# Kernel tuning notes

Measured on AMD Instinct MI355X. Metric: run time of the kernel, lower is better.

The kernel has to match this reference:

```python
import jax, jax.numpy as jnp
import numpy as np

HEAD_SIZE = 64
N_EMBD = 768

def setup_inputs() -> dict:
    key = jax.random.key(0)
    k1, k2, k3, k4 = jax.random.split(key, 4)
    x = jax.random.normal(k1, (8, 2048, N_EMBD), dtype=jnp.float32)
    # nn.Linear weights are [out, in]; we store transposed [in, out] for x @ W
    scale = 1.0 / np.sqrt(N_EMBD)
    Wk = jax.random.uniform(k2, (N_EMBD, HEAD_SIZE), jnp.float32, -scale, scale)
    Wq = jax.random.uniform(k3, (N_EMBD, HEAD_SIZE), jnp.float32, -scale, scale)
    Wv = jax.random.uniform(k4, (N_EMBD, HEAD_SIZE), jnp.float32, -scale, scale)
    return {"x": x, "Wk": Wk, "Wq": Wq, "Wv": Wv}

def reference(x, Wk, Wq, Wv):
    # x: [B, T, C]
    k = x @ Wk  # [B, T, H]
    q = x @ Wq  # [B, T, H]
    v = x @ Wv  # [B, T, H]
    inv_sqrt_h = jnp.asarray(k.shape[-1], x.dtype) ** -0.5
    att = jnp.einsum('bth,bsh->bts', q, k) * inv_sqrt_h  # [B, T, T]
    att = jax.nn.softmax(att, axis=-1)  # no causal mask in original
    out = jnp.einsum('bts,bsh->bth', att, v)  # [B, T, H]
    return out
```

## Files before the change

### kernel.cpp

```cpp
#include <hip/hip_runtime.h>
#include <hip/hip_bf16.h>


#define SEQ   2048
#define CEMB  768
#define SCL 0.18033688011112042f
#define THR 11.0f

typedef __attribute__((ext_vector_type(4))) float f32x4;
typedef __attribute__((ext_vector_type(4))) float fvec4;
typedef __attribute__((ext_vector_type(8))) short short8;
typedef __attribute__((ext_vector_type(4))) short short4v;
typedef __attribute__((ext_vector_type(4))) unsigned short u16x4;
typedef __attribute__((ext_vector_type(8))) unsigned short u16x8;
typedef __attribute__((ext_vector_type(2))) unsigned int u32x2;

#define MFMA32 __builtin_amdgcn_mfma_f32_16x16x32_bf16

__device__ __forceinline__ unsigned short f2bf(float f) {
    unsigned int u = __builtin_bit_cast(unsigned int, f);
    u += 0x7fffu + ((u >> 16) & 1u);
    return (unsigned short)(u >> 16);
}
__device__ __forceinline__ float bf2f(unsigned short s) {
    return __builtin_bit_cast(float, (unsigned int)s << 16);
}
__device__ __forceinline__ unsigned int pack_bf2(float lo, float hi) {
    unsigned int ulo = __builtin_bit_cast(unsigned int, lo);
    unsigned int uhi = __builtin_bit_cast(unsigned int, hi);
    return ((uhi + 0x8000u) & 0xffff0000u) | ((ulo + 0x8000u) >> 16);
}
__device__ __forceinline__ short8 pack8(fvec4 a, fvec4 b) {
    short8 s;
    #pragma unroll
    for (int j = 0; j < 4; ++j) {
        s[j]     = (short)f2bf(a[j]);
        s[4 + j] = (short)f2bf(b[j]);
    }
    return s;
}
__device__ __forceinline__ f32x4 vmax4(f32x4 a, f32x4 b) {
    f32x4 r;
    r[0] = fmaxf(a[0], b[0]); r[1] = fmaxf(a[1], b[1]);
    r[2] = fmaxf(a[2], b[2]); r[3] = fmaxf(a[3], b[3]);
    return r;
}
__device__ __forceinline__ void gl_lds16(const void* g, void* l) {
    __builtin_amdgcn_global_load_lds(
        (const __attribute__((address_space(1))) unsigned int*)g,
        (__attribute__((address_space(3))) unsigned int*)l, 16, 0, 0);
}

__global__ void wt_kernel(const float* __restrict__ Wq, const float* __restrict__ Wk,
                          const float* __restrict__ Wv, unsigned short* __restrict__ wt) {
    int idx = blockIdx.x * 256 + threadIdx.x;
    int o = idx / 49152;
    int r = idx % 49152;
    int n = r / 768;
    int k = r % 768;
    const float* W = (o == 0) ? Wq : (o == 1) ? Wk : Wv;
    wt[idx] = f2bf(W[k * 64 + n]);
}

__global__ __launch_bounds__(768) void proj_kernel(
        const float* __restrict__ x, const unsigned short* __restrict__ wt,
        unsigned short* __restrict__ qg, unsigned short* __restrict__ kg,
        unsigned short* __restrict__ vtg) {
    __shared__ __align__(16) unsigned short xl[2][12288];

    const int tid = threadIdx.x;
    const int lane = tid & 63;
    const int wv = tid >> 6;
    const int l15 = lane & 15;
    const int lq = lane >> 4;
    const int o = wv >> 2;
    const int f = wv & 3;
    const int rowbase = blockIdx.x * 64;

    short8 wfr[24];
    #pragma unroll
    for (int s = 0; s < 24; ++s)
        wfr[s] = *reinterpret_cast<const short8*>(
            &wt[o * 49152 + (f * 16 + l15) * CEMB + s * 32 + lq * 8]);

    const int S0 = tid, S1 = 768 + tid;
    const int r0 = S0 / 96, c0 = S0 - r0 * 96;
    const int r1 = S1 / 96, c1 = S1 - r1 * 96;
    const int d0 = r0 * 1536 + ((c0 ^ (r0 & 7)) << 4);
    const int d1 = r1 * 1536 + ((c1 ^ (r1 & 7)) << 4);

    #define LOADT(PA0, PA1, PB0, PB1, T) do {                               \
        const float* g0_ = x + (size_t)(rowbase + (T) * 16 + r0) * CEMB + c0 * 8; \
        const float* g1_ = x + (size_t)(rowbase + (T) * 16 + r1) * CEMB + c1 * 8; \
        PA0 = *reinterpret_cast<const fvec4*>(g0_);                         \
        PA1 = *reinterpret_cast<const fvec4*>(g0_ + 4);                     \
        PB0 = *reinterpret_cast<const fvec4*>(g1_);                         \
        PB1 = *reinterpret_cast<const fvec4*>(g1_ + 4);                     \
    } while (0)

    fvec4 pb[2][4];
    {
        fvec4 a0, a1, b0, b1;
        LOADT(a0, a1, b0, b1, 0);
        *reinterpret_cast<short8*>((char*)&xl[0][0] + d0) = pack8(a0, a1);
        *reinterpret_cast<short8*>((char*)&xl[0][0] + d1) = pack8(b0, b1);
        LOADT(pb[0][0], pb[0][1], pb[0][2], pb[0][3], 1);
    }
    __syncthreads();

    #pragma unroll
    for (int t = 0; t < 4; ++t) {
        const int cur = t & 1;
        if (t < 2)
            LOADT(pb[cur ^ 1][0], pb[cur ^ 1][1], pb[cur ^ 1][2], pb[cur ^ 1][3], t + 2);

        f32x4 acc = f32x4{0.f, 0.f, 0.f, 0.f};
        const char* xb = (const char*)&xl[cur][0];
        const int rswz = l15 & 7;
        #pragma unroll
        for (int s = 0; s < 24; ++s) {
            short8 bf = *reinterpret_cast<const short8*>(
                xb + l15 * 1536 + (((s * 4 + lq) ^ rswz) << 4));
            acc = MFMA32(wfr[s], bf, acc, 0, 0, 0);
        }

        if (t < 3) {
            *reinterpret_cast<short8*>((char*)&xl[cur ^ 1][0] + d0) =
                pack8(pb[cur][0], pb[cur][1]);
            *reinterpret_cast<short8*>((char*)&xl[cur ^ 1][0] + d1) =
                pack8(pb[cur][2], pb[cur][3]);
        }

        const int xrow = rowbase + t * 16 + l15;
        if (o < 2) {
            const float sc = o ? 1.f : SCL;
            u16x4 st;
            #pragma unroll
            for (int r = 0; r < 4; ++r) st[r] = f2bf(acc[r] * sc);
            unsigned short* dst = (o ? kg : qg) + (size_t)xrow * 64 + f * 16 + lq * 4;
            *reinterpret_cast<u16x4*>(dst) = st;
        } else {
            const int bb = xrow >> 11;
            const int tt = xrow & 2047;
            #pragma unroll
            for (int r = 0; r < 4; ++r)
                vtg[(size_t)bb * 131072 + (size_t)(f * 16 + lq * 4 + r) * SEQ + tt] =
                    f2bf(acc[r]);
        }
        __syncthreads();
    }
    #undef LOADT
}

#if __has_builtin(__builtin_amdgcn_mfma_f32_16x16x16bf16_1k)
#define HAVE_MFMA16 1
#define MFMA16 __builtin_amdgcn_mfma_f32_16x16x16bf16_1k
#else
#define HAVE_MFMA16 0
#endif

__global__ __launch_bounds__(256) void attn_kernel(
        const unsigned short* __restrict__ qg, const unsigned short* __restrict__ kg,
        const unsigned short* __restrict__ vtg, unsigned short* __restrict__ pO,
        float* __restrict__ pm, float* __restrict__ pl) {
    __shared__ __align__(16) unsigned short kbuf[2][4096];
    __shared__ __align__(16) unsigned short vbuf[2][4096];

    const int tid = threadIdx.x;
    const int lane = tid & 63;
    const int wv = tid >> 6;
    const int l15 = lane & 15;
    const int lq = lane >> 4;

    const int swz = (blockIdx.x & 7) * 64 + (blockIdx.x >> 3);
    const int b = swz >> 6;
    const int qt = (swz >> 2) & 15;
    const int ks = swz & 3;
    const int qrow0 = b * SEQ + qt * 128 + wv * 32;

    const unsigned short* kgb = kg + (size_t)(b * SEQ + ks * 512) * 64;
    const unsigned short* vgb = vtg + (size_t)b * 131072 + ks * 512;

    const int sr0 = tid >> 3;
    const int sw0 = (((tid & 7) ^ (sr0 & 7)) * 8);
    const int sr1 = 32 + sr0;
    const int sw1 = (((tid & 7) ^ (sr1 & 7)) * 8);
    #define STAGE(S, KT) do {                                                        \
        gl_lds16(kgb + (size_t)((KT) * 64 + sr0) * 64 + sw0, &kbuf[S][tid * 8]);       \
        gl_lds16(kgb + (size_t)((KT) * 64 + sr1) * 64 + sw1, &kbuf[S][2048 + tid * 8]); \
        gl_lds16(vgb + (size_t)sr0 * SEQ + (KT) * 64 + sw0, &vbuf[S][tid * 8]);        \
        gl_lds16(vgb + (size_t)sr1 * SEQ + (KT) * 64 + sw1, &vbuf[S][2048 + tid * 8]);  \
    } while (0)

    const short8 bq00 = *reinterpret_cast<const short8*>(&qg[(size_t)(qrow0 + l15) * 64 + lq * 8]);
    const short8 bq01 = *reinterpret_cast<const short8*>(&qg[(size_t)(qrow0 + l15) * 64 + 32 + lq * 8]);
    const short8 bq10 = *reinterpret_cast<const short8*>(&qg[(size_t)(qrow0 + 16 + l15) * 64 + lq * 8]);
    const short8 bq11 = *reinterpret_cast<const short8*>(&qg[(size_t)(qrow0 + 16 + l15) * 64 + 32 + lq * 8]);

    f32x4 acc0[4], acc1[4];
    #pragma unroll
    for (int hb = 0; hb < 4; ++hb) {
        acc0[hb] = f32x4{0.f, 0.f, 0.f, 0.f};
        acc1[hb] = f32x4{0.f, 0.f, 0.f, 0.f};
    }
    float m0 = -3e38f, m1 = -3e38f, l0 = 0.f, l1 = 0.f;

    STAGE(0, 0);
    __syncthreads();

    #define SUBITER(BQ0, BQ1, MM, LL, ACC) do {                                      \
        f32x4 st[4];                                                                 \
        _Pragma("unroll")                                                            \
        for (int kb = 0; kb < 4; ++kb) {                                             \
            f32x4 z = {0.f, 0.f, 0.f, 0.f};                                          \
            st[kb] = MFMA32(kf[2 * kb], BQ0, z, 0, 0, 0);                            \
            st[kb] = MFMA32(kf[2 * kb + 1], BQ1, st[kb], 0, 0, 0);                   \
        }                                                                            \
        f32x4 mx = vmax4(vmax4(st[0], st[1]), vmax4(st[2], st[3]));                  \
        float p = fmaxf(fmaxf(mx[0], mx[1]), fmaxf(mx[2], mx[3]));                   \
        p = fmaxf(p, __shfl_xor(p, 16)); p = fmaxf(p, __shfl_xor(p, 32));            \
        if (__any(p > MM + THR)) {                                                   \
            float mn = fmaxf(MM, p);                                                 \
            float al = exp2f(MM - mn);                                               \
            MM = mn; LL *= al;                                                       \
            _Pragma("unroll")                                                        \
            for (int hb = 0; hb < 4; ++hb)                                           \
                _Pragma("unroll")                                                    \
                for (int r = 0; r < 4; ++r) ACC[hb][r] *= al;                        \
        }                                                                            \
        unsigned int w[4][2];                                                        \
        _Pragma("unroll")                                                            \
        for (int kb = 0; kb < 4; ++kb) {                                             \
            float e0 = exp2f(st[kb][0] - MM), e1 = exp2f(st[kb][1] - MM);            \
            float e2 = exp2f(st[kb][2] - MM), e3 = exp2f(st[kb][3] - MM);            \
            LL += (e0 + e1) + (e2 + e3);                                             \
            w[kb][0] = pack_bf2(e0, e1); w[kb][1] = pack_bf2(e2, e3);                \
        }                                                                            \
        PVACC_L(w, ACC);                                                             \
    } while (0)

#if HAVE_MFMA16
    #define PVLOAD_L                                                                 \
        short4v va[16];                                                              \
        _Pragma("unroll")                                                            \
        for (int hb = 0; hb < 4; ++hb) {                                             \
            const int row = hb * 16 + l15, rs = row & 7, rb = row * 128;             \
            _Pragma("unroll")                                                        \
            for (int kb = 0; kb < 4; ++kb)                                           \
                va[hb * 4 + kb] = *reinterpret_cast<const short4v*>(                 \
                    vb_ + rb + (((kb * 2 + (lq >> 1)) ^ rs) << 4) + (lq & 1) * 8);   \
        }
    #define PVACC_L(W, ACC) do {                                                     \
        _Pragma("unroll")                                                            \
        for (int hb = 0; hb < 4; ++hb) {                                             \
            f32x4 a = ACC[hb];                                                       \
            _Pragma("unroll")                                                        \
            for (int kb = 0; kb < 4; ++kb) {                                         \
                u32x2 uv; uv[0] = W[kb][0]; uv[1] = W[kb][1];                        \
                a = MFMA16(va[hb * 4 + kb], __builtin_bit_cast(short4v, uv), a, 0, 0, 0); \
            }                                                                        \
            ACC[hb] = a;                                                             \
        }                                                                            \
    } while (0)
#else
    #define PVLOAD_L                                                                 \
        short8 va[8];                                                                \
        _Pragma("unroll")                                                            \
        for (int hb = 0; hb < 4; ++hb) {                                             \
            const int row = hb * 16 + l15, rs = row & 7, rb = row * 128;             \
            _Pragma("unroll")                                                        \
            for (int h = 0; h < 2; ++h)                                              \
                va[hb * 2 + h] = *reinterpret_cast<const short8*>(                   \
                    vb_ + rb + (((h * 4 + lq) ^ rs) << 4));                          \
        }
    #define PVACC_L(W, ACC) do {                                                     \
        _Pragma("unroll")                                                            \
        for (int h = 0; h < 2; ++h) {                                                \
            unsigned int bw0, bw1, bw2, bw3;                                         \
            {                                                                        \
                int src0 = l15 + (((lq & 1) * 2) << 4);                              \
                int src1 = l15 + ((((lq & 1) * 2) + 1) << 4);                        \
                unsigned int a0 = (unsigned int)__shfl((int)W[h * 2][0], src0);      \
                unsigned int a1 = (unsigned int)__shfl((int)W[h * 2 + 1][0], src0);  \
                unsigned int b0 = (unsigned int)__shfl((int)W[h * 2][1], src0);      \
                unsigned int b1 = (unsigned int)__shfl((int)W[h * 2 + 1][1], src0);  \
                unsigned int c0_ = (unsigned int)__shfl((int)W[h * 2][0], src1);     \
                unsigned int c1_ = (unsigned int)__shfl((int)W[h * 2 + 1][0], src1); \
                unsigned int d0_ = (unsigned int)__shfl((int)W[h * 2][1], src1);     \
                unsigned int d1_ = (unsigned int)__shfl((int)W[h * 2 + 1][1], src1); \
                bw0 = (lq >> 1) ? a1 : a0; bw1 = (lq >> 1) ? b1 : b0;                \
                bw2 = (lq >> 1) ? c1_ : c0_; bw3 = (lq >> 1) ? d1_ : d0_;            \
            }                                                                        \
            short8 bp;                                                               \
            {                                                                        \
                unsigned int t_[4] = {bw0, bw2, bw1, bw3};                           \
                bp = *reinterpret_cast<short8*>(t_);                                 \
            }                                                                        \
            _Pragma("unroll")                                                        \
            for (int hb = 0; hb < 4; ++hb)                                           \
                ACC[hb] = MFMA32(va[hb * 2 + h], bp, ACC[hb], 0, 0, 0);              \
        }                                                                            \
    } while (0)
#endif

    #define ITERL(S) do {                                                            \
        const char* kb_ = (const char*)&kbuf[S][0];                                  \
        const char* vb_ = (const char*)&vbuf[S][0];                                  \
        short8 kf[8];                                                                \
        _Pragma("unroll")                                                            \
        for (int kb = 0; kb < 4; ++kb) {                                             \
            const int row = kb * 16 + l15, rs = row & 7, rb = row * 128;             \
            kf[2 * kb]     = *reinterpret_cast<const short8*>(kb_ + rb + ((lq ^ rs) << 4));       \
            kf[2 * kb + 1] = *reinterpret_cast<const short8*>(kb_ + rb + (((lq + 4) ^ rs) << 4)); \
        }                                                                            \
        PVLOAD_L;                                                                    \
        SUBITER(bq00, bq01, m0, l0, acc0);                                           \
        SUBITER(bq10, bq11, m1, l1, acc1);                                           \
    } while (0)

    #pragma unroll
    for (int kt2 = 0; kt2 < 4; ++kt2) {
        const int t0 = kt2 * 2;
        if (t0 + 1 < 8) STAGE(1, t0 + 1);
        ITERL(0);
        __syncthreads();
        if (t0 + 2 < 8) STAGE(0, t0 + 2);
        ITERL(1);
        __syncthreads();
    }

    l0 += __shfl_xor(l0, 16); l0 += __shfl_xor(l0, 32);
    l1 += __shfl_xor(l1, 16); l1 += __shfl_xor(l1, 32);

    #pragma unroll
    for (int s = 0; s < 2; ++s) {
        const int q = qrow0 + s * 16 + l15;
        f32x4* ac = s ? acc1 : acc0;
        #pragma unroll
        for (int hb = 0; hb < 4; ++hb) {
            u16x4 st;
            #pragma unroll
            for (int r = 0; r < 4; ++r) st[r] = f2bf(ac[hb][r]);
            *reinterpret_cast<u16x4*>(&pO[((size_t)(ks * 16384 + q)) * 64 + hb * 16 + lq * 4]) = st;
        }
        pm[ks * 16384 + q] = s ? m1 : m0;
        pl[ks * 16384 + q] = s ? l1 : l0;
    }
    #undef STAGE
    #undef ITERL
    #undef SUBITER
    #undef PVLOAD_L
    #undef PVACC_L
}

__global__ __launch_bounds__(256) void combine_kernel(
        float* __restrict__ out, const unsigned short* __restrict__ pO,
        const float* __restrict__ pm, const float* __restrict__ pl) {
    const int idx = blockIdx.x * 256 + threadIdx.x;
    const int q = idx >> 2;
    const int c0 = (idx & 3) * 16;

    float mv[4], lv[4];
    #pragma unroll
    for (int k = 0; k < 4; ++k) {
        mv[k] = pm[k * 16384 + q];
        lv[k] = pl[k * 16384 + q];
    }
    float M = fmaxf(fmaxf(mv[0], mv[1]), fmaxf(mv[2], mv[3]));
    float e[4], L = 0.f;
    #pragma unroll
    for (int k = 0; k < 4; ++k) {
        e[k] = exp2f(mv[k] - M);
        L += lv[k] * e[k];
    }
    const float inv = 1.0f / L;

    float res[16];
    #pragma unroll
    for (int j = 0; j < 16; ++j) res[j] = 0.f;
    #pragma unroll
    for (int k = 0; k < 4; ++k) {
        const unsigned short* p = &pO[((size_t)(k * 16384 + q)) * 64 + c0];
        u16x8 a = *reinterpret_cast<const u16x8*>(p);
        u16x8 b = *reinterpret_cast<const u16x8*>(p + 8);
        #pragma unroll
        for (int j = 0; j < 8; ++j) {
            res[j]     += e[k] * bf2f(a[j]);
            res[8 + j] += e[k] * bf2f(b[j]);
        }
    }
    float* op = &out[(size_t)q * 64 + c0];
    #pragma unroll
    for (int v = 0; v < 4; ++v) {
        fvec4 r;
        #pragma unroll
        for (int j = 0; j < 4; ++j) r[j] = res[v * 4 + j] * inv;
        *reinterpret_cast<fvec4*>(op + v * 4) = r;
    }
}

extern "C" void kernel_launch(void* const* d_in, const int* in_sizes, int n_in,
                              void* d_out, int out_size, void* d_ws, size_t ws_size,
                              hipStream_t stream) {
    (void)in_sizes; (void)n_in; (void)out_size; (void)ws_size;
    const float* x  = (const float*)d_in[0];
    const float* Wk = (const float*)d_in[1];
    const float* Wq = (const float*)d_in[2];
    const float* Wv = (const float*)d_in[3];
    float* out = (float*)d_out;

    unsigned short* ws = (unsigned short*)d_ws;
    unsigned short* qg  = ws;
    unsigned short* kg  = ws + 1048576;
    unsigned short* vtg = ws + 2097152;
    unsigned short* wt  = ws + 3145728;
    float* pm = (float*)((char*)d_ws + 6586368);
    float* pl = pm + 65536;
    unsigned short* pO = (unsigned short*)((char*)d_ws + 7110656);

    wt_kernel<<<576, 256, 0, stream>>>(Wq, Wk, Wv, wt);
    proj_kernel<<<256, 768, 0, stream>>>(x, wt, qg, kg, vtg);
    attn_kernel<<<512, 256, 0, stream>>>(qg, kg, vtg, pO, pm, pl);
    combine_kernel<<<256, 256, 0, stream>>>(out, pO, pm, pl);
}
```

Before: 55.11 us.

## Fuse weight conversion into projection and split-K combine into attention kernel

Removes the separate weight-transpose kernel: each projection block now loads the fp32 weights directly with strided scalar reads and converts them to bf16 in registers. It also removes the separate combine kernel. The last of the four key-split attention blocks for each query tile, found with an atomic counter and threadfences, merges the partial outputs in place. This saves two kernel launches and their inter-kernel gaps, at the cost of uncoalesced weight reads repeated by every projection block and a serialized tail of combine work in the last-arriving blocks.

```diff
diff --git a/kernel.cpp b/kernel.cpp
--- a/kernel.cpp
+++ b/kernel.cpp
@@ -51,21 +51,11 @@
         (__attribute__((address_space(3))) unsigned int*)l, 16, 0, 0);
 }
 
-__global__ void wt_kernel(const float* __restrict__ Wq, const float* __restrict__ Wk,
-                          const float* __restrict__ Wv, unsigned short* __restrict__ wt) {
-    int idx = blockIdx.x * 256 + threadIdx.x;
-    int o = idx / 49152;
-    int r = idx % 49152;
-    int n = r / 768;
-    int k = r % 768;
-    const float* W = (o == 0) ? Wq : (o == 1) ? Wk : Wv;
-    wt[idx] = f2bf(W[k * 64 + n]);
-}
-
 __global__ __launch_bounds__(768) void proj_kernel(
-        const float* __restrict__ x, const unsigned short* __restrict__ wt,
+        const float* __restrict__ x, const float* __restrict__ Wq,
+        const float* __restrict__ Wk, const float* __restrict__ Wv,
         unsigned short* __restrict__ qg, unsigned short* __restrict__ kg,
-        unsigned short* __restrict__ vtg) {
+        unsigned short* __restrict__ vtg, unsigned int* __restrict__ cnt) {
     __shared__ __align__(16) unsigned short xl[2][12288];
 
     const int tid = threadIdx.x;
@@ -77,11 +67,18 @@
     const int f = wv & 3;
     const int rowbase = blockIdx.x * 64;
 
+    if (blockIdx.x == 0 && tid < 128) cnt[tid] = 0u;
+
+    const float* Wsrc = (o == 0) ? Wq : (o == 1) ? Wk : Wv;
+    const float* wp0 = Wsrc + (size_t)(lq * 8) * 64 + (f * 16 + l15);
     short8 wfr[24];
     #pragma unroll
-    for (int s = 0; s < 24; ++s)
-        wfr[s] = *reinterpret_cast<const short8*>(
-            &wt[o * 49152 + (f * 16 + l15) * CEMB + s * 32 + lq * 8]);
+    for (int s = 0; s < 24; ++s) {
+        const float* wp = wp0 + (size_t)s * 32 * 64;
+        #pragma unroll
+        for (int j = 0; j < 8; ++j)
+            wfr[s][j] = (short)f2bf(wp[j * 64]);
+    }
 
     const int S0 = tid, S1 = 768 + tid;
     const int r0 = S0 / 96, c0 = S0 - r0 * 96;
@@ -162,9 +159,11 @@
 __global__ __launch_bounds__(256) void attn_kernel(
         const unsigned short* __restrict__ qg, const unsigned short* __restrict__ kg,
         const unsigned short* __restrict__ vtg, unsigned short* __restrict__ pO,
-        float* __restrict__ pm, float* __restrict__ pl) {
+        float* __restrict__ pm, float* __restrict__ pl,
+        unsigned int* __restrict__ cnt, float* __restrict__ out) {
     __shared__ __align__(16) unsigned short kbuf[2][4096];
     __shared__ __align__(16) unsigned short vbuf[2][4096];
+    __shared__ unsigned int lastflag;
 
     const int tid = threadIdx.x;
     const int lane = tid & 63;
@@ -351,51 +350,58 @@
     #undef SUBITER
     #undef PVLOAD_L
     #undef PVACC_L
-}
-
-__global__ __launch_bounds__(256) void combine_kernel(
-        float* __restrict__ out, const unsigned short* __restrict__ pO,
-        const float* __restrict__ pm, const float* __restrict__ pl) {
-    const int idx = blockIdx.x * 256 + threadIdx.x;
-    const int q = idx >> 2;
-    const int c0 = (idx & 3) * 16;
-
-    float mv[4], lv[4];
-    #pragma unroll
-    for (int k = 0; k < 4; ++k) {
-        mv[k] = pm[k * 16384 + q];
-        lv[k] = pl[k * 16384 + q];
-    }
-    float M = fmaxf(fmaxf(mv[0], mv[1]), fmaxf(mv[2], mv[3]));
-    float e[4], L = 0.f;
-    #pragma unroll
-    for (int k = 0; k < 4; ++k) {
-        e[k] = exp2f(mv[k] - M);
-        L += lv[k] * e[k];
-    }
-    const float inv = 1.0f / L;
-
-    float res[16];
-    #pragma unroll
-    for (int j = 0; j < 16; ++j) res[j] = 0.f;
-    #pragma unroll
-    for (int k = 0; k < 4; ++k) {
-        const unsigned short* p = &pO[((size_t)(k * 16384 + q)) * 64 + c0];
-        u16x8 a = *reinterpret_cast<const u16x8*>(p);
-        u16x8 b = *reinterpret_cast<const u16x8*>(p + 8);
-        #pragma unroll
-        for (int j = 0; j < 8; ++j) {
-            res[j]     += e[k] * bf2f(a[j]);
-            res[8 + j] += e[k] * bf2f(b[j]);
-        }
-    }
-    float* op = &out[(size_t)q * 64 + c0];
-    #pragma unroll
-    for (int v = 0; v < 4; ++v) {
-        fvec4 r;
-        #pragma unroll
-        for (int j = 0; j < 4; ++j) r[j] = res[v * 4 + j] * inv;
-        *reinterpret_cast<fvec4*>(op + v * 4) = r;
+
+    __threadfence();
+    if (tid == 0) {
+        unsigned int old = atomicAdd(&cnt[b * 16 + qt], 1u);
+        lastflag = (old == 3u) ? 1u : 0u;
+    }
+    __syncthreads();
+    if (lastflag) {
+        __threadfence();
+        const int qbase = b * SEQ + qt * 128;
+        #pragma unroll 2
+        for (int it = tid; it < 512; it += 256) {
+            const int row = it >> 2;
+            const int c0 = (it & 3) * 16;
+            const int q = qbase + row;
+            float mv[4], lv[4];
+            #pragma unroll
+            for (int k = 0; k < 4; ++k) {
+                mv[k] = pm[k * 16384 + q];
+                lv[k] = pl[k * 16384 + q];
+            }
+            float M = fmaxf(fmaxf(mv[0], mv[1]), fmaxf(mv[2], mv[3]));
+            float e[4], L = 0.f;
+            #pragma unroll
+            for (int k = 0; k < 4; ++k) {
+                e[k] = exp2f(mv[k] - M);
+                L += lv[k] * e[k];
+            }
+            const float inv = 1.0f / L;
+            float res[16];
+            #pragma unroll
+            for (int j = 0; j < 16; ++j) res[j] = 0.f;
+            #pragma unroll
+            for (int k = 0; k < 4; ++k) {
+                const unsigned short* p = &pO[((size_t)(k * 16384 + q)) * 64 + c0];
+                u16x8 a = *reinterpret_cast<const u16x8*>(p);
+                u16x8 bvec = *reinterpret_cast<const u16x8*>(p + 8);
+                #pragma unroll
+                for (int j = 0; j < 8; ++j) {
+                    res[j]     += e[k] * bf2f(a[j]);
+                    res[8 + j] += e[k] * bf2f(bvec[j]);
+                }
+            }
+            float* op = &out[(size_t)q * 64 + c0];
+            #pragma unroll
+            for (int v = 0; v < 4; ++v) {
+                fvec4 r;
+                #pragma unroll
+                for (int j = 0; j < 4; ++j) r[j] = res[v * 4 + j] * inv;
+                *reinterpret_cast<fvec4*>(op + v * 4) = r;
+            }
+        }
     }
 }
 
@@ -413,13 +419,11 @@
     unsigned short* qg  = ws;
     unsigned short* kg  = ws + 1048576;
     unsigned short* vtg = ws + 2097152;
-    unsigned short* wt  = ws + 3145728;
+    unsigned int* cnt = (unsigned int*)((char*)d_ws + 6291456);
     float* pm = (float*)((char*)d_ws + 6586368);
     float* pl = pm + 65536;
     unsigned short* pO = (unsigned short*)((char*)d_ws + 7110656);
 
-    wt_kernel<<<576, 256, 0, stream>>>(Wq, Wk, Wv, wt);
-    proj_kernel<<<256, 768, 0, stream>>>(x, wt, qg, kg, vtg);
-    attn_kernel<<<512, 256, 0, stream>>>(qg, kg, vtg, pO, pm, pl);
-    combine_kernel<<<256, 256, 0, stream>>>(out, pO, pm, pl);
-}
+    proj_kernel<<<256, 768, 0, stream>>>(x, Wq, Wk, Wv, qg, kg, vtg, cnt);
+    attn_kernel<<<512, 256, 0, stream>>>(qg, kg, vtg, pO, pm, pl, cnt, out);
+}
```

After: 140.7 us. 2.55x slower.

## Fuse weight prep, projection, attention and combine into one cooperative kernel

Applied to the files above, without the earlier changes.

Replaces the four separate kernel launches with one cooperative kernel of 256 blocks x 768 threads. Grid-wide syncs separate the weight transpose, QKV projection, split-K attention and combine phases. The goal is to remove launch overhead and the gaps between kernels. In exchange the attention phase runs with only 256 blocks of 768 threads, where it previously used 512 blocks of 256. Some waves idle through matching __syncthreads calls, and grid.sync adds its own barrier cost.

```diff
diff --git a/kernel.cpp b/kernel.cpp
--- a/kernel.cpp
+++ b/kernel.cpp
@@ -1,5 +1,8 @@
 #include <hip/hip_runtime.h>
 #include <hip/hip_bf16.h>
+#include <hip/hip_cooperative_groups.h>
+
+namespace cg = cooperative_groups;
 
 
 #define SEQ   2048
@@ -51,107 +54,6 @@
         (__attribute__((address_space(3))) unsigned int*)l, 16, 0, 0);
 }
 
-__global__ void wt_kernel(const float* __restrict__ Wq, const float* __restrict__ Wk,
-                          const float* __restrict__ Wv, unsigned short* __restrict__ wt) {
-    int idx = blockIdx.x * 256 + threadIdx.x;
-    int o = idx / 49152;
-    int r = idx % 49152;
-    int n = r / 768;
-    int k = r % 768;
-    const float* W = (o == 0) ? Wq : (o == 1) ? Wk : Wv;
-    wt[idx] = f2bf(W[k * 64 + n]);
-}
-
-__global__ __launch_bounds__(768) void proj_kernel(
-        const float* __restrict__ x, const unsigned short* __restrict__ wt,
-        unsigned short* __restrict__ qg, unsigned short* __restrict__ kg,
-        unsigned short* __restrict__ vtg) {
-    __shared__ __align__(16) unsigned short xl[2][12288];
-
-    const int tid = threadIdx.x;
-    const int lane = tid & 63;
-    const int wv = tid >> 6;
-    const int l15 = lane & 15;
-    const int lq = lane >> 4;
-    const int o = wv >> 2;
-    const int f = wv & 3;
-    const int rowbase = blockIdx.x * 64;
-
-    short8 wfr[24];
-    #pragma unroll
-    for (int s = 0; s < 24; ++s)
-        wfr[s] = *reinterpret_cast<const short8*>(
-            &wt[o * 49152 + (f * 16 + l15) * CEMB + s * 32 + lq * 8]);
-
-    const int S0 = tid, S1 = 768 + tid;
-    const int r0 = S0 / 96, c0 = S0 - r0 * 96;
-    const int r1 = S1 / 96, c1 = S1 - r1 * 96;
-    const int d0 = r0 * 1536 + ((c0 ^ (r0 & 7)) << 4);
-    const int d1 = r1 * 1536 + ((c1 ^ (r1 & 7)) << 4);
-
-    #define LOADT(PA0, PA1, PB0, PB1, T) do {                               \
-        const float* g0_ = x + (size_t)(rowbase + (T) * 16 + r0) * CEMB + c0 * 8; \
-        const float* g1_ = x + (size_t)(rowbase + (T) * 16 + r1) * CEMB + c1 * 8; \
-        PA0 = *reinterpret_cast<const fvec4*>(g0_);                         \
-        PA1 = *reinterpret_cast<const fvec4*>(g0_ + 4);                     \
-        PB0 = *reinterpret_cast<const fvec4*>(g1_);                         \
-        PB1 = *reinterpret_cast<const fvec4*>(g1_ + 4);                     \
-    } while (0)
-
-    fvec4 pb[2][4];
-    {
-        fvec4 a0, a1, b0, b1;
-        LOADT(a0, a1, b0, b1, 0);
-        *reinterpret_cast<short8*>((char*)&xl[0][0] + d0) = pack8(a0, a1);
-        *reinterpret_cast<short8*>((char*)&xl[0][0] + d1) = pack8(b0, b1);
-        LOADT(pb[0][0], pb[0][1], pb[0][2], pb[0][3], 1);
-    }
-    __syncthreads();
-
-    #pragma unroll
-    for (int t = 0; t < 4; ++t) {
-        const int cur = t & 1;
-        if (t < 2)
-            LOADT(pb[cur ^ 1][0], pb[cur ^ 1][1], pb[cur ^ 1][2], pb[cur ^ 1][3], t + 2);
-
-        f32x4 acc = f32x4{0.f, 0.f, 0.f, 0.f};
-        const char* xb = (const char*)&xl[cur][0];
-        const int rswz = l15 & 7;
-        #pragma unroll
-        for (int s = 0; s < 24; ++s) {
-            short8 bf = *reinterpret_cast<const short8*>(
-                xb + l15 * 1536 + (((s * 4 + lq) ^ rswz) << 4));
-            acc = MFMA32(wfr[s], bf, acc, 0, 0, 0);
-        }
-
-        if (t < 3) {
-            *reinterpret_cast<short8*>((char*)&xl[cur ^ 1][0] + d0) =
-                pack8(pb[cur][0], pb[cur][1]);
-            *reinterpret_cast<short8*>((char*)&xl[cur ^ 1][0] + d1) =
-                pack8(pb[cur][2], pb[cur][3]);
-        }
-
-        const int xrow = rowbase + t * 16 + l15;
-        if (o < 2) {
-            const float sc = o ? 1.f : SCL;
-            u16x4 st;
-            #pragma unroll
-            for (int r = 0; r < 4; ++r) st[r] = f2bf(acc[r] * sc);
-            unsigned short* dst = (o ? kg : qg) + (size_t)xrow * 64 + f * 16 + lq * 4;
-            *reinterpret_cast<u16x4*>(dst) = st;
-        } else {
-            const int bb = xrow >> 11;
-            const int tt = xrow & 2047;
-            #pragma unroll
-            for (int r = 0; r < 4; ++r)
-                vtg[(size_t)bb * 131072 + (size_t)(f * 16 + lq * 4 + r) * SEQ + tt] =
-                    f2bf(acc[r]);
-        }
-        __syncthreads();
-    }
-    #undef LOADT
-}
-
 #if __has_builtin(__builtin_amdgcn_mfma_f32_16x16x16bf16_1k)
 #define HAVE_MFMA16 1
 #define MFMA16 __builtin_amdgcn_mfma_f32_16x16x16bf16_1k
@@ -159,243 +61,362 @@
 #define HAVE_MFMA16 0
 #endif
 
-__global__ __launch_bounds__(256) void attn_kernel(
-        const unsigned short* __restrict__ qg, const unsigned short* __restrict__ kg,
-        const unsigned short* __restrict__ vtg, unsigned short* __restrict__ pO,
-        float* __restrict__ pm, float* __restrict__ pl) {
-    __shared__ __align__(16) unsigned short kbuf[2][4096];
-    __shared__ __align__(16) unsigned short vbuf[2][4096];
-
+__global__ __launch_bounds__(768) void fused_kernel(
+        const float* __restrict__ x, const float* __restrict__ Wq,
+        const float* __restrict__ Wk, const float* __restrict__ Wv,
+        unsigned short* __restrict__ wt, unsigned short* __restrict__ qg,
+        unsigned short* __restrict__ kg, unsigned short* __restrict__ vtg,
+        unsigned short* __restrict__ pO, float* __restrict__ pm,
+        float* __restrict__ pl, float* __restrict__ out) {
+    __shared__ __align__(16) unsigned short smem[32768];
+
+    cg::grid_group grid = cg::this_grid();
     const int tid = threadIdx.x;
-    const int lane = tid & 63;
-    const int wv = tid >> 6;
-    const int l15 = lane & 15;
-    const int lq = lane >> 4;
-
-    const int swz = (blockIdx.x & 7) * 64 + (blockIdx.x >> 3);
-    const int b = swz >> 6;
-    const int qt = (swz >> 2) & 15;
-    const int ks = swz & 3;
-    const int qrow0 = b * SEQ + qt * 128 + wv * 32;
-
-    const unsigned short* kgb = kg + (size_t)(b * SEQ + ks * 512) * 64;
-    const unsigned short* vgb = vtg + (size_t)b * 131072 + ks * 512;
-
-    const int sr0 = tid >> 3;
-    const int sw0 = (((tid & 7) ^ (sr0 & 7)) * 8);
-    const int sr1 = 32 + sr0;
-    const int sw1 = (((tid & 7) ^ (sr1 & 7)) * 8);
-    #define STAGE(S, KT) do {                                                        \
-        gl_lds16(kgb + (size_t)((KT) * 64 + sr0) * 64 + sw0, &kbuf[S][tid * 8]);       \
-        gl_lds16(kgb + (size_t)((KT) * 64 + sr1) * 64 + sw1, &kbuf[S][2048 + tid * 8]); \
-        gl_lds16(vgb + (size_t)sr0 * SEQ + (KT) * 64 + sw0, &vbuf[S][tid * 8]);        \
-        gl_lds16(vgb + (size_t)sr1 * SEQ + (KT) * 64 + sw1, &vbuf[S][2048 + tid * 8]);  \
-    } while (0)
-
-    const short8 bq00 = *reinterpret_cast<const short8*>(&qg[(size_t)(qrow0 + l15) * 64 + lq * 8]);
-    const short8 bq01 = *reinterpret_cast<const short8*>(&qg[(size_t)(qrow0 + l15) * 64 + 32 + lq * 8]);
-    const short8 bq10 = *reinterpret_cast<const short8*>(&qg[(size_t)(qrow0 + 16 + l15) * 64 + lq * 8]);
-    const short8 bq11 = *reinterpret_cast<const short8*>(&qg[(size_t)(qrow0 + 16 + l15) * 64 + 32 + lq * 8]);
-
-    f32x4 acc0[4], acc1[4];
-    #pragma unroll
-    for (int hb = 0; hb < 4; ++hb) {
-        acc0[hb] = f32x4{0.f, 0.f, 0.f, 0.f};
-        acc1[hb] = f32x4{0.f, 0.f, 0.f, 0.f};
-    }
-    float m0 = -3e38f, m1 = -3e38f, l0 = 0.f, l1 = 0.f;
-
-    STAGE(0, 0);
-    __syncthreads();
-
-    #define SUBITER(BQ0, BQ1, MM, LL, ACC) do {                                      \
-        f32x4 st[4];                                                                 \
-        _Pragma("unroll")                                                            \
-        for (int kb = 0; kb < 4; ++kb) {                                             \
-            f32x4 z = {0.f, 0.f, 0.f, 0.f};                                          \
-            st[kb] = MFMA32(kf[2 * kb], BQ0, z, 0, 0, 0);                            \
-            st[kb] = MFMA32(kf[2 * kb + 1], BQ1, st[kb], 0, 0, 0);                   \
-        }                                                                            \
-        f32x4 mx = vmax4(vmax4(st[0], st[1]), vmax4(st[2], st[3]));                  \
-        float p = fmaxf(fmaxf(mx[0], mx[1]), fmaxf(mx[2], mx[3]));                   \
-        p = fmaxf(p, __shfl_xor(p, 16)); p = fmaxf(p, __shfl_xor(p, 32));            \
-        if (__any(p > MM + THR)) {                                                   \
-            float mn = fmaxf(MM, p);                                                 \
-            float al = exp2f(MM - mn);                                               \
-            MM = mn; LL *= al;                                                       \
-            _Pragma("unroll")                                                        \
-            for (int hb = 0; hb < 4; ++hb)                                           \
-                _Pragma("unroll")                                                    \
-                for (int r = 0; r < 4; ++r) ACC[hb][r] *= al;                        \
-        }                                                                            \
-        unsigned int w[4][2];                                                        \
-        _Pragma("unroll")                                                            \
-        for (int kb = 0; kb < 4; ++kb) {                                             \
-            float e0 = exp2f(st[kb][0] - MM), e1 = exp2f(st[kb][1] - MM);            \
-            float e2 = exp2f(st[kb][2] - MM), e3 = exp2f(st[kb][3] - MM);            \
-            LL += (e0 + e1) + (e2 + e3);                                             \
-            w[kb][0] = pack_bf2(e0, e1); w[kb][1] = pack_bf2(e2, e3);                \
-        }                                                                            \
-        PVACC_L(w, ACC);                                                             \
-    } while (0)
-
-#if HAVE_MFMA16
-    #define PVLOAD_L                                                                 \
-        short4v va[16];                                                              \
-        _Pragma("unroll")                                                            \
-        for (int hb = 0; hb < 4; ++hb) {                                             \
-            const int row = hb * 16 + l15, rs = row & 7, rb = row * 128;             \
-            _Pragma("unroll")                                                        \
-            for (int kb = 0; kb < 4; ++kb)                                           \
-                va[hb * 4 + kb] = *reinterpret_cast<const short4v*>(                 \
-                    vb_ + rb + (((kb * 2 + (lq >> 1)) ^ rs) << 4) + (lq & 1) * 8);   \
-        }
-    #define PVACC_L(W, ACC) do {                                                     \
-        _Pragma("unroll")                                                            \
-        for (int hb = 0; hb < 4; ++hb) {                                             \
-            f32x4 a = ACC[hb];                                                       \
-            _Pragma("unroll")                                                        \
-            for (int kb = 0; kb < 4; ++kb) {                                         \
-                u32x2 uv; uv[0] = W[kb][0]; uv[1] = W[kb][1];                        \
-                a = MFMA16(va[hb * 4 + kb], __builtin_bit_cast(short4v, uv), a, 0, 0, 0); \
-            }                                                                        \
-            ACC[hb] = a;                                                             \
-        }                                                                            \
-    } while (0)
-#else
-    #define PVLOAD_L                                                                 \
-        short8 va[8];                                                                \
-        _Pragma("unroll")                                                            \
-        for (int hb = 0; hb < 4; ++hb) {                                             \
-            const int row = hb * 16 + l15, rs = row & 7, rb = row * 128;             \
-            _Pragma("unroll")                                                        \
-            for (int h = 0; h < 2; ++h)                                              \
-                va[hb * 2 + h] = *reinterpret_cast<const short8*>(                   \
-                    vb_ + rb + (((h * 4 + lq) ^ rs) << 4));                          \
-        }
-    #define PVACC_L(W, ACC) do {                                                     \
-        _Pragma("unroll")                                                            \
-        for (int h = 0; h < 2; ++h) {                                                \
-            unsigned int bw0, bw1, bw2, bw3;                                         \
-            {                                                                        \
-                int src0 = l15 + (((lq & 1) * 2) << 4);                              \
-                int src1 = l15 + ((((lq & 1) * 2) + 1) << 4);                        \
-                unsigned int a0 = (unsigned int)__shfl((int)W[h * 2][0], src0);      \
-                unsigned int a1 = (unsigned int)__shfl((int)W[h * 2 + 1][0], src0);  \
-                unsigned int b0 = (unsigned int)__shfl((int)W[h * 2][1], src0);      \
-                unsigned int b1 = (unsigned int)__shfl((int)W[h * 2 + 1][1], src0);  \
-                unsigned int c0_ = (unsigned int)__shfl((int)W[h * 2][0], src1);     \
-                unsigned int c1_ = (unsigned int)__shfl((int)W[h * 2 + 1][0], src1); \
-                unsigned int d0_ = (unsigned int)__shfl((int)W[h * 2][1], src1);     \
-                unsigned int d1_ = (unsigned int)__shfl((int)W[h * 2 + 1][1], src1); \
-                bw0 = (lq >> 1) ? a1 : a0; bw1 = (lq >> 1) ? b1 : b0;                \
-                bw2 = (lq >> 1) ? c1_ : c0_; bw3 = (lq >> 1) ? d1_ : d0_;            \
-            }                                                                        \
-            short8 bp;                                                               \
-            {                                                                        \
-                unsigned int t_[4] = {bw0, bw2, bw1, bw3};                           \
-                bp = *reinterpret_cast<short8*>(t_);                                 \
-            }                                                                        \
-            _Pragma("unroll")                                                        \
-            for (int hb = 0; hb < 4; ++hb)                                           \
-                ACC[hb] = MFMA32(va[hb * 2 + h], bp, ACC[hb], 0, 0, 0);              \
-        }                                                                            \
-    } while (0)
-#endif
-
-    #define ITERL(S) do {                                                            \
-        const char* kb_ = (const char*)&kbuf[S][0];                                  \
-        const char* vb_ = (const char*)&vbuf[S][0];                                  \
-        short8 kf[8];                                                                \
-        _Pragma("unroll")                                                            \
-        for (int kb = 0; kb < 4; ++kb) {                                             \
-            const int row = kb * 16 + l15, rs = row & 7, rb = row * 128;             \
-            kf[2 * kb]     = *reinterpret_cast<const short8*>(kb_ + rb + ((lq ^ rs) << 4));       \
-            kf[2 * kb + 1] = *reinterpret_cast<const short8*>(kb_ + rb + (((lq + 4) ^ rs) << 4)); \
-        }                                                                            \
-        PVLOAD_L;                                                                    \
-        SUBITER(bq00, bq01, m0, l0, acc0);                                           \
-        SUBITER(bq10, bq11, m1, l1, acc1);                                           \
-    } while (0)
-
-    #pragma unroll
-    for (int kt2 = 0; kt2 < 4; ++kt2) {
-        const int t0 = kt2 * 2;
-        if (t0 + 1 < 8) STAGE(1, t0 + 1);
-        ITERL(0);
-        __syncthreads();
-        if (t0 + 2 < 8) STAGE(0, t0 + 2);
-        ITERL(1);
-        __syncthreads();
-    }
-
-    l0 += __shfl_xor(l0, 16); l0 += __shfl_xor(l0, 32);
-    l1 += __shfl_xor(l1, 16); l1 += __shfl_xor(l1, 32);
-
-    #pragma unroll
-    for (int s = 0; s < 2; ++s) {
-        const int q = qrow0 + s * 16 + l15;
-        f32x4* ac = s ? acc1 : acc0;
-        #pragma unroll
-        for (int hb = 0; hb < 4; ++hb) {
-            u16x4 st;
-            #pragma unroll
-            for (int r = 0; r < 4; ++r) st[r] = f2bf(ac[hb][r]);
-            *reinterpret_cast<u16x4*>(&pO[((size_t)(ks * 16384 + q)) * 64 + hb * 16 + lq * 4]) = st;
-        }
-        pm[ks * 16384 + q] = s ? m1 : m0;
-        pl[ks * 16384 + q] = s ? l1 : l0;
-    }
-    #undef STAGE
-    #undef ITERL
-    #undef SUBITER
-    #undef PVLOAD_L
-    #undef PVACC_L
-}
-
-__global__ __launch_bounds__(256) void combine_kernel(
-        float* __restrict__ out, const unsigned short* __restrict__ pO,
-        const float* __restrict__ pm, const float* __restrict__ pl) {
-    const int idx = blockIdx.x * 256 + threadIdx.x;
-    const int q = idx >> 2;
-    const int c0 = (idx & 3) * 16;
-
-    float mv[4], lv[4];
-    #pragma unroll
-    for (int k = 0; k < 4; ++k) {
-        mv[k] = pm[k * 16384 + q];
-        lv[k] = pl[k * 16384 + q];
-    }
-    float M = fmaxf(fmaxf(mv[0], mv[1]), fmaxf(mv[2], mv[3]));
-    float e[4], L = 0.f;
-    #pragma unroll
-    for (int k = 0; k < 4; ++k) {
-        e[k] = exp2f(mv[k] - M);
-        L += lv[k] * e[k];
-    }
-    const float inv = 1.0f / L;
-
-    float res[16];
-    #pragma unroll
-    for (int j = 0; j < 16; ++j) res[j] = 0.f;
-    #pragma unroll
-    for (int k = 0; k < 4; ++k) {
-        const unsigned short* p = &pO[((size_t)(k * 16384 + q)) * 64 + c0];
-        u16x8 a = *reinterpret_cast<const u16x8*>(p);
-        u16x8 b = *reinterpret_cast<const u16x8*>(p + 8);
-        #pragma unroll
-        for (int j = 0; j < 8; ++j) {
-            res[j]     += e[k] * bf2f(a[j]);
-            res[8 + j] += e[k] * bf2f(b[j]);
+    const int bid = blockIdx.x;
+
+    {
+        int idx = bid * 768 + tid;
+        if (idx < 147456) {
+            int o = idx / 49152;
+            int r = idx % 49152;
+            int n = r / 768;
+            int k = r % 768;
+            const float* W = (o == 0) ? Wq : (o == 1) ? Wk : Wv;
+            wt[idx] = f2bf(W[k * 64 + n]);
         }
     }
-    float* op = &out[(size_t)q * 64 + c0];
-    #pragma unroll
-    for (int v = 0; v < 4; ++v) {
-        fvec4 r;
+    grid.sync();
+
+    {
+        unsigned short (*xl)[12288] = reinterpret_cast<unsigned short (*)[12288]>(&smem[0]);
+        const int lane = tid & 63;
+        const int wv = tid >> 6;
+        const int l15 = lane & 15;
+        const int lq = lane >> 4;
+        const int o = wv >> 2;
+        const int f = wv & 3;
+        const int rowbase = bid * 64;
+
+        short8 wfr[24];
         #pragma unroll
-        for (int j = 0; j < 4; ++j) r[j] = res[v * 4 + j] * inv;
-        *reinterpret_cast<fvec4*>(op + v * 4) = r;
+        for (int s = 0; s < 24; ++s)
+            wfr[s] = *reinterpret_cast<const short8*>(
+                &wt[o * 49152 + (f * 16 + l15) * CEMB + s * 32 + lq * 8]);
+
+        const int S0 = tid, S1 = 768 + tid;
+        const int r0 = S0 / 96, c0 = S0 - r0 * 96;
+        const int r1 = S1 / 96, c1 = S1 - r1 * 96;
+        const int d0 = r0 * 1536 + ((c0 ^ (r0 & 7)) << 4);
+        const int d1 = r1 * 1536 + ((c1 ^ (r1 & 7)) << 4);
+
+        #define LOADT(PA0, PA1, PB0, PB1, T) do {                               \
+            const float* g0_ = x + (size_t)(rowbase + (T) * 16 + r0) * CEMB + c0 * 8; \
+            const float* g1_ = x + (size_t)(rowbase + (T) * 16 + r1) * CEMB + c1 * 8; \
+            PA0 = *reinterpret_cast<const fvec4*>(g0_);                         \
+            PA1 = *reinterpret_cast<const fvec4*>(g0_ + 4);                     \
+            PB0 = *reinterpret_cast<const fvec4*>(g1_);                         \
+            PB1 = *reinterpret_cast<const fvec4*>(g1_ + 4);                     \
+        } while (0)
+
+        fvec4 pb[2][4];
+        {
+            fvec4 a0, a1, b0, b1;
+            LOADT(a0, a1, b0, b1, 0);
+            *reinterpret_cast<short8*>((char*)&xl[0][0] + d0) = pack8(a0, a1);
+            *reinterpret_cast<short8*>((char*)&xl[0][0] + d1) = pack8(b0, b1);
+            LOADT(pb[0][0], pb[0][1], pb[0][2], pb[0][3], 1);
+        }
+        __syncthreads();
+
+        #pragma unroll
+        for (int t = 0; t < 4; ++t) {
+            const int cur = t & 1;
+            if (t < 2)
+                LOADT(pb[cur ^ 1][0], pb[cur ^ 1][1], pb[cur ^ 1][2], pb[cur ^ 1][3], t + 2);
+
+            f32x4 acc = f32x4{0.f, 0.f, 0.f, 0.f};
+            const char* xb = (const char*)&xl[cur][0];
+            const int rswz = l15 & 7;
+            #pragma unroll
+            for (int s = 0; s < 24; ++s) {
+                short8 bf = *reinterpret_cast<const short8*>(
+                    xb + l15 * 1536 + (((s * 4 + lq) ^ rswz) << 4));
+                acc = MFMA32(wfr[s], bf, acc, 0, 0, 0);
+            }
+
+            if (t < 3) {
+                *reinterpret_cast<short8*>((char*)&xl[cur ^ 1][0] + d0) =
+                    pack8(pb[cur][0], pb[cur][1]);
+                *reinterpret_cast<short8*>((char*)&xl[cur ^ 1][0] + d1) =
+                    pack8(pb[cur][2], pb[cur][3]);
+            }
+
+            const int xrow = rowbase + t * 16 + l15;
+            if (o < 2) {
+                const float sc = o ? 1.f : SCL;
+                u16x4 st;
+                #pragma unroll
+                for (int r = 0; r < 4; ++r) st[r] = f2bf(acc[r] * sc);
+                unsigned short* dst = (o ? kg : qg) + (size_t)xrow * 64 + f * 16 + lq * 4;
+                *reinterpret_cast<u16x4*>(dst) = st;
+            } else {
+                const int bb = xrow >> 11;
+                const int tt = xrow & 2047;
+                #pragma unroll
+                for (int r = 0; r < 4; ++r)
+                    vtg[(size_t)bb * 131072 + (size_t)(f * 16 + lq * 4 + r) * SEQ + tt] =
+                        f2bf(acc[r]);
+            }
+            __syncthreads();
+        }
+        #undef LOADT
+    }
+    grid.sync();
+
+    {
+        const int wg = tid >> 8;
+        const int t256 = tid & 255;
+
+        if (wg < 2) {
+            unsigned short* base = &smem[wg * 16384];
+            const int b = bid & 7;
+            const int combo = (bid >> 3) * 2 + wg;
+            const int qt = combo >> 2;
+            const int ks = combo & 3;
+            const int lane = t256 & 63;
+            const int wv = t256 >> 6;
+            const int l15 = lane & 15;
+            const int lq = lane >> 4;
+            const int qrow0 = b * SEQ + qt * 128 + wv * 32;
+
+            const unsigned short* kgb = kg + (size_t)(b * SEQ + ks * 512) * 64;
+            const unsigned short* vgb = vtg + (size_t)b * 131072 + ks * 512;
+
+            const int sr0 = t256 >> 3;
+            const int sw0 = (((t256 & 7) ^ (sr0 & 7)) * 8);
+            const int sr1 = 32 + sr0;
+            const int sw1 = (((t256 & 7) ^ (sr1 & 7)) * 8);
+            #define KBUF(S) (base + (S) * 4096)
+            #define VBUF(S) (base + 8192 + (S) * 4096)
+            #define STAGE(S, KT) do {                                                    \
+                gl_lds16(kgb + (size_t)((KT) * 64 + sr0) * 64 + sw0, KBUF(S) + t256 * 8);  \
+                gl_lds16(kgb + (size_t)((KT) * 64 + sr1) * 64 + sw1, KBUF(S) + 2048 + t256 * 8); \
+                gl_lds16(vgb + (size_t)sr0 * SEQ + (KT) * 64 + sw0, VBUF(S) + t256 * 8);   \
+                gl_lds16(vgb + (size_t)sr1 * SEQ + (KT) * 64 + sw1, VBUF(S) + 2048 + t256 * 8);  \
+            } while (0)
+
+            const short8 bq00 = *reinterpret_cast<const short8*>(&qg[(size_t)(qrow0 + l15) * 64 + lq * 8]);
+            const short8 bq01 = *reinterpret_cast<const short8*>(&qg[(size_t)(qrow0 + l15) * 64 + 32 + lq * 8]);
+            const short8 bq10 = *reinterpret_cast<const short8*>(&qg[(size_t)(qrow0 + 16 + l15) * 64 + lq * 8]);
+            const short8 bq11 = *reinterpret_cast<const short8*>(&qg[(size_t)(qrow0 + 16 + l15) * 64 + 32 + lq * 8]);
+
+            f32x4 acc0[4], acc1[4];
+            #pragma unroll
+            for (int hb = 0; hb < 4; ++hb) {
+                acc0[hb] = f32x4{0.f, 0.f, 0.f, 0.f};
+                acc1[hb] = f32x4{0.f, 0.f, 0.f, 0.f};
+            }
+            float m0 = -3e38f, m1 = -3e38f, l0 = 0.f, l1 = 0.f;
+
+            STAGE(0, 0);
+            __syncthreads();
+
+            #define SUBITER(BQ0, BQ1, MM, LL, ACC) do {                                      \
+                f32x4 st[4];                                                                 \
+                _Pragma("unroll")                                                            \
+                for (int kb = 0; kb < 4; ++kb) {                                             \
+                    f32x4 z = {0.f, 0.f, 0.f, 0.f};                                          \
+                    st[kb] = MFMA32(kf[2 * kb], BQ0, z, 0, 0, 0);                            \
+                    st[kb] = MFMA32(kf[2 * kb + 1], BQ1, st[kb], 0, 0, 0);                   \
+                }                                                                            \
+                f32x4 mx = vmax4(vmax4(st[0], st[1]), vmax4(st[2], st[3]));                  \
+                float p = fmaxf(fmaxf(mx[0], mx[1]), fmaxf(mx[2], mx[3]));                   \
+                p = fmaxf(p, __shfl_xor(p, 16)); p = fmaxf(p, __shfl_xor(p, 32));            \
+                if (__any(p > MM + THR)) {                                                   \
+                    float mn = fmaxf(MM, p);                                                 \
+                    float al = exp2f(MM - mn);                                               \
+                    MM = mn; LL *= al;                                                       \
+                    _Pragma("unroll")                                                        \
+                    for (int hb = 0; hb < 4; ++hb)                                           \
+                        _Pragma("unroll")                                                    \
+                        for (int r = 0; r < 4; ++r) ACC[hb][r] *= al;                        \
+                }                                                                            \
+                unsigned int w[4][2];                                                        \
+                _Pragma("unroll")                                                            \
+                for (int kb = 0; kb < 4; ++kb) {                                             \
+                    float e0 = exp2f(st[kb][0] - MM), e1 = exp2f(st[kb][1] - MM);            \
+                    float e2 = exp2f(st[kb][2] - MM), e3 = exp2f(st[kb][3] - MM);            \
+                    LL += (e0 + e1) + (e2 + e3);                                             \
+                    w[kb][0] = pack_bf2(e0, e1); w[kb][1] = pack_bf2(e2, e3);                \
+                }                                                                            \
+                PVACC_L(w, ACC);                                                             \
+            } while (0)
+
+#if HAVE_MFMA16
+            #define PVLOAD_L                                                                 \
+                short4v va[16];                                                              \
+                _Pragma("unroll")                                                            \
+                for (int hb = 0; hb < 4; ++hb) {                                             \
+                    const int row = hb * 16 + l15, rs = row & 7, rb = row * 128;             \
+                    _Pragma("unroll")                                                        \
+                    for (int kb = 0; kb < 4; ++kb)                                           \
+                        va[hb * 4 + kb] = *reinterpret_cast<const short4v*>(                 \
+                            vb_ + rb + (((kb * 2 + (lq >> 1)) ^ rs) << 4) + (lq & 1) * 8);   \
+                }
+            #define PVACC_L(W, ACC) do {                                                     \
+                _Pragma("unroll")                                                            \
+                for (int hb = 0; hb < 4; ++hb) {                                             \
+                    f32x4 a = ACC[hb];                                                       \
+                    _Pragma("unroll")                                                        \
+                    for (int kb = 0; kb < 4; ++kb) {                                         \
+                        u32x2 uv; uv[0] = W[kb][0]; uv[1] = W[kb][1];                        \
+                        a = MFMA16(va[hb * 4 + kb], __builtin_bit_cast(short4v, uv), a, 0, 0, 0); \
+                    }                                                                        \
+                    ACC[hb] = a;                                                             \
+                }                                                                            \
+            } while (0)
+#else
+            #define PVLOAD_L                                                                 \
+                short8 va[8];                                                                \
+                _Pragma("unroll")                                                            \
+                for (int hb = 0; hb < 4; ++hb) {                                             \
+                    const int row = hb * 16 + l15, rs = row & 7, rb = row * 128;             \
+                    _Pragma("unroll")                                                        \
+                    for (int h = 0; h < 2; ++h)                                              \
+                        va[hb * 2 + h] = *reinterpret_cast<const short8*>(                   \
+                            vb_ + rb + (((h * 4 + lq) ^ rs) << 4));                          \
+                }
+            #define PVACC_L(W, ACC) do {                                                     \
+                _Pragma("unroll")                                                            \
+                for (int h = 0; h < 2; ++h) {                                                \
+                    unsigned int bw0, bw1, bw2, bw3;                                         \
+                    {                                                                        \
+                        int src0 = l15 + (((lq & 1) * 2) << 4);                              \
+                        int src1 = l15 + ((((lq & 1) * 2) + 1) << 4);                        \
+                        unsigned int a0 = (unsigned int)__shfl((int)W[h * 2][0], src0);      \
+                        unsigned int a1 = (unsigned int)__shfl((int)W[h * 2 + 1][0], src0);  \
+                        unsigned int b0 = (unsigned int)__shfl((int)W[h * 2][1], src0);      \
+                        unsigned int b1 = (unsigned int)__shfl((int)W[h * 2 + 1][1], src0);  \
+                        unsigned int c0_ = (unsigned int)__shfl((int)W[h * 2][0], src1);     \
+                        unsigned int c1_ = (unsigned int)__shfl((int)W[h * 2 + 1][0], src1); \
+                        unsigned int d0_ = (unsigned int)__shfl((int)W[h * 2][1], src1);     \
+                        unsigned int d1_ = (unsigned int)__shfl((int)W[h * 2 + 1][1], src1); \
+                        bw0 = (lq >> 1) ? a1 : a0; bw1 = (lq >> 1) ? b1 : b0;                \
+                        bw2 = (lq >> 1) ? c1_ : c0_; bw3 = (lq >> 1) ? d1_ : d0_;            \
+                    }                                                                        \
+                    short8 bp;                                                               \
+                    {                                                                        \
+                        unsigned int t_[4] = {bw0, bw2, bw1, bw3};                           \
+                        bp = *reinterpret_cast<short8*>(t_);                                 \
+                    }                                                                        \
+                    _Pragma("unroll")                                                        \
+                    for (int hb = 0; hb < 4; ++hb)                                           \
+                        ACC[hb] = MFMA32(va[hb * 2 + h], bp, ACC[hb], 0, 0, 0);              \
+                }                                                                            \
+            } while (0)
+#endif
+
+            #define ITERL(S) do {                                                            \
+                const char* kb_ = (const char*)KBUF(S);                                      \
+                const char* vb_ = (const char*)VBUF(S);                                      \
+                short8 kf[8];                                                                \
+                _Pragma("unroll")                                                            \
+                for (int kb = 0; kb < 4; ++kb) {                                             \
+                    const int row = kb * 16 + l15, rs = row & 7, rb = row * 128;             \
+                    kf[2 * kb]     = *reinterpret_cast<const short8*>(kb_ + rb + ((lq ^ rs) << 4));       \
+                    kf[2 * kb + 1] = *reinterpret_cast<const short8*>(kb_ + rb + (((lq + 4) ^ rs) << 4)); \
+                }                                                                            \
+                PVLOAD_L;                                                                    \
+                SUBITER(bq00, bq01, m0, l0, acc0);                                           \
+                SUBITER(bq10, bq11, m1, l1, acc1);                                           \
+            } while (0)
+
+            #pragma unroll
+            for (int kt2 = 0; kt2 < 4; ++kt2) {
+                const int t0 = kt2 * 2;
+                if (t0 + 1 < 8) STAGE(1, t0 + 1);
+                ITERL(0);
+                __syncthreads();
+                if (t0 + 2 < 8) STAGE(0, t0 + 2);
+                ITERL(1);
+                __syncthreads();
+            }
+
+            l0 += __shfl_xor(l0, 16); l0 += __shfl_xor(l0, 32);
+            l1 += __shfl_xor(l1, 16); l1 += __shfl_xor(l1, 32);
+
+            #pragma unroll
+            for (int s = 0; s < 2; ++s) {
+                const int q = qrow0 + s * 16 + l15;
+                f32x4* ac = s ? acc1 : acc0;
+                #pragma unroll
+                for (int hb = 0; hb < 4; ++hb) {
+                    u16x4 st;
+                    #pragma unroll
+                    for (int r = 0; r < 4; ++r) st[r] = f2bf(ac[hb][r]);
+                    *reinterpret_cast<u16x4*>(&pO[((size_t)(ks * 16384 + q)) * 64 + hb * 16 + lq * 4]) = st;
+                }
+                pm[ks * 16384 + q] = s ? m1 : m0;
+                pl[ks * 16384 + q] = s ? l1 : l0;
+            }
+            #undef STAGE
+            #undef ITERL
+            #undef SUBITER
+            #undef PVLOAD_L
+            #undef PVACC_L
+            #undef KBUF
+            #undef VBUF
+        } else {
+            #pragma unroll
+            for (int i = 0; i < 9; ++i) __syncthreads();
+        }
+    }
+    grid.sync();
+
+    {
+        const int idx = bid * 768 + tid;
+        if (idx < 65536) {
+            const int q = idx >> 2;
+            const int c0 = (idx & 3) * 16;
+
+            float mv[4], lv[4];
+            #pragma unroll
+            for (int k = 0; k < 4; ++k) {
+                mv[k] = pm[k * 16384 + q];
+                lv[k] = pl[k * 16384 + q];
+            }
+            float M = fmaxf(fmaxf(mv[0], mv[1]), fmaxf(mv[2], mv[3]));
+            float e[4], L = 0.f;
+            #pragma unroll
+            for (int k = 0; k < 4; ++k) {
+                e[k] = exp2f(mv[k] - M);
+                L += lv[k] * e[k];
+            }
+            const float inv = 1.0f / L;
+
+            float res[16];
+            #pragma unroll
+            for (int j = 0; j < 16; ++j) res[j] = 0.f;
+            #pragma unroll
+            for (int k = 0; k < 4; ++k) {
+                const unsigned short* p = &pO[((size_t)(k * 16384 + q)) * 64 + c0];
+                u16x8 a = *reinterpret_cast<const u16x8*>(p);
+                u16x8 bvec = *reinterpret_cast<const u16x8*>(p + 8);
+                #pragma unroll
+                for (int j = 0; j < 8; ++j) {
+                    res[j]     += e[k] * bf2f(a[j]);
+                    res[8 + j] += e[k] * bf2f(bvec[j]);
+                }
+            }
+            float* op = &out[(size_t)q * 64 + c0];
+            #pragma unroll
+            for (int v = 0; v < 4; ++v) {
+                fvec4 r;
+                #pragma unroll
+                for (int j = 0; j < 4; ++j) r[j] = res[v * 4 + j] * inv;
+                *reinterpret_cast<fvec4*>(op + v * 4) = r;
+            }
+        }
     }
 }
 
@@ -418,8 +439,11 @@
     float* pl = pm + 65536;
     unsigned short* pO = (unsigned short*)((char*)d_ws + 7110656);
 
-    wt_kernel<<<576, 256, 0, stream>>>(Wq, Wk, Wv, wt);
-    proj_kernel<<<256, 768, 0, stream>>>(x, wt, qg, kg, vtg);
-    attn_kernel<<<512, 256, 0, stream>>>(qg, kg, vtg, pO, pm, pl);
-    combine_kernel<<<256, 256, 0, stream>>>(out, pO, pm, pl);
-}
+    void* args[] = {
+        (void*)&x, (void*)&Wq, (void*)&Wk, (void*)&Wv,
+        (void*)&wt, (void*)&qg, (void*)&kg, (void*)&vtg,
+        (void*)&pO, (void*)&pm, (void*)&pl, (void*)&out
+    };
+    hipLaunchCooperativeKernel((void*)fused_kernel, dim3(256), dim3(768),
+                               args, 0, stream);
+}
```

New measurement: 165.7 us. +200.7%, slower.
